# Optimization experiments

Hardware: AMD Instinct MI355X
Metric: run time of the kernel (lower is better)

## Reference

```python
import jax, jax.numpy as jnp
import numpy as np

N_NODES = 100000
N_EDGES = 1600000
IN_FEATS = 64
HIDDEN = 64
TOPO_DIM = 16
NUM_CLASSES = 4
NUM_GRAPHS = 64


def setup_inputs() -> dict:
    key = jax.random.key(0)
    ks = jax.random.split(key, 10)
    x = jax.random.normal(ks[0], (N_NODES, IN_FEATS), dtype=jnp.float32)
    edge_index = jax.random.randint(ks[1], (2, N_EDGES), 0, N_NODES, dtype=jnp.int64)
    batch = jnp.sort(jax.random.randint(ks[2], (N_NODES,), 0, NUM_GRAPHS, dtype=jnp.int64))
    topo = jax.random.normal(ks[3], (NUM_GRAPHS, TOPO_DIM), dtype=jnp.float32)
    # GCNConv weights (glorot-ish scale) and biases
    W1 = jax.random.normal(ks[4], (IN_FEATS, HIDDEN), dtype=jnp.float32) / np.sqrt(IN_FEATS)
    b1 = jnp.zeros((HIDDEN,), dtype=jnp.float32)
    W2 = jax.random.normal(ks[5], (HIDDEN, HIDDEN), dtype=jnp.float32) / np.sqrt(HIDDEN)
    b2 = jnp.zeros((HIDDEN,), dtype=jnp.float32)
    Wlin = jax.random.normal(ks[6], (HIDDEN + TOPO_DIM, NUM_CLASSES), dtype=jnp.float32) / np.sqrt(HIDDEN + TOPO_DIM)
    blin = jnp.zeros((NUM_CLASSES,), dtype=jnp.float32)
    return {"x": x, "edge_index": edge_index, "batch": batch, "topo": topo,
            "W1": W1, "b1": b1, "W2": W2, "b2": b2, "Wlin": Wlin, "blin": blin}


def _gcn_conv(x, W, b, src, dst, deg_inv_sqrt):
    # PyG GCNConv: add self-loops, symmetric normalization D^-1/2 (A+I) D^-1/2, then linear.
    xw = x @ W                                   # [N, H]
    norm = deg_inv_sqrt[src] * deg_inv_sqrt[dst]  # [E]
    msgs = xw[src] * norm[:, None]               # gather + scale, [E, H]
    agg = jax.ops.segment_sum(msgs, dst, num_segments=x.shape[0])
    # self-loop contribution: norm_ii = deg_inv_sqrt[i]^2
    agg = agg + xw * (deg_inv_sqrt * deg_inv_sqrt)[:, None]
    return agg + b


def reference(x, edge_index, batch, topo, W1, b1, W2, b2, Wlin, blin):
    src, dst = edge_index[0], edge_index[1]
    n = x.shape[0]
    # degree including self-loop
    deg = jax.ops.segment_sum(jnp.ones_like(dst, dtype=x.dtype), dst, num_segments=n) + 1.0
    deg_inv_sqrt = jax.lax.rsqrt(deg)
    h = jax.nn.relu(_gcn_conv(x, W1, b1, src, dst, deg_inv_sqrt))
    # F.dropout(p=0.5, training=False) -> identity at inference
    h = jax.nn.relu(_gcn_conv(h, W2, b2, src, dst, deg_inv_sqrt))
    # global mean pool over graphs
    sums = jax.ops.segment_sum(h, batch, num_segments=NUM_GRAPHS)
    counts = jax.ops.segment_sum(jnp.ones((n,), dtype=h.dtype), batch, num_segments=NUM_GRAPHS)
    g = sums / jnp.maximum(counts, 1.0)[:, None]  # [G, H]
    gtopo = jnp.concatenate([g, topo], axis=1)    # [G, H + topo_dim]
    return gtopo @ Wlin + blin
```

## Files before the change

### kernel.cpp

```cpp
#include <hip/hip_runtime.h>
#include <hip/hip_bf16.h>

#define NGRAPH  64
#define TOPO_D  16
#define NBLK    512
#define MAXB    512
#define GROWS   8

typedef float v2f __attribute__((ext_vector_type(2)));

static __device__ __forceinline__ unsigned f2bf(float f) {
    unsigned u = __float_as_uint(f);
    return (u + 0x7FFFu + ((u >> 16) & 1u)) >> 16;
}
static __device__ __forceinline__ float bf_lo(unsigned u) { return __uint_as_float(u << 16); }
static __device__ __forceinline__ float bf_hi(unsigned u) { return __uint_as_float(u & 0xFFFF0000u); }

static __device__ __forceinline__ void gemm_rows_bf(
        const float* __restrict__ X, const float* Wreg,
        unsigned short* __restrict__ Abf, int row0, int N, int lane) {
    #pragma unroll
    for (int j = 0; j < GROWS; ++j) {
        int row = row0 + j;
        if (row >= N) return;
        const float* xr = X + (size_t)row * 64;
        float acc = 0.0f;
        #pragma unroll
        for (int k = 0; k < 64; ++k) acc = fmaf(xr[k], Wreg[k], acc);
        Abf[(size_t)row * 64 + lane] = (unsigned short)f2bf(acc);
    }
}

static __device__ __forceinline__ void gemm_rows_fp8(
        const unsigned* __restrict__ X32, const float* Wreg,
        unsigned* __restrict__ A8, const float* __restrict__ dis,
        int row0, int N, int lane) {
    #pragma unroll
    for (int j = 0; j < GROWS; ++j) {
        int row = row0 + j;
        if (row >= N) return;
        const unsigned* xr = X32 + (size_t)row * 32;
        float acc = 0.0f;
        #pragma unroll
        for (int k = 0; k < 32; ++k) {
            unsigned u = xr[k];
            acc = fmaf(bf_lo(u), Wreg[2 * k], acc);
            acc = fmaf(bf_hi(u), Wreg[2 * k + 1], acc);
        }
        acc *= dis[row];
        float nb1 = __shfl_xor(acc, 1, 64);
        float lo = (lane & 1) ? nb1 : acc;
        float hi = (lane & 1) ? acc : nb1;
        int pk = __builtin_amdgcn_cvt_pk_fp8_f32(lo, hi, 0, false);
        int pk2 = __shfl_xor(pk, 2, 64);
        unsigned dw = (lane & 2) ? (((unsigned)pk2 & 0xFFFFu) | ((unsigned)pk << 16))
                                 : (((unsigned)pk & 0xFFFFu) | ((unsigned)pk2 << 16));
        if ((lane & 3) == 0) A8[(size_t)row * 16 + (lane >> 2)] = dw;
    }
}

__global__ __launch_bounds__(256) void hybrid_gemm_hist_kernel(
        const float* __restrict__ X, const float* __restrict__ W,
        unsigned short* __restrict__ Abf,
        const int* __restrict__ dst, int* __restrict__ bhist,
        int N, int E, int Gg, int nb2, int CE) {
    __shared__ int hist[MAXB];
    int t = threadIdx.x;
    if ((int)blockIdx.x < Gg) {
        int lane = t & 63;
        float Wreg[64];
        #pragma unroll
        for (int k = 0; k < 64; ++k) Wreg[k] = W[k * 64 + lane];
        int wave = __builtin_amdgcn_readfirstlane(blockIdx.x * 4 + (t >> 6));
        gemm_rows_bf(X, Wreg, Abf, wave * GROWS, N, lane);
    } else {
        int blk = blockIdx.x - Gg;
        for (int i = t; i < nb2; i += 256) hist[i] = 0;
        __syncthreads();
        int e0 = blk * CE, e1 = min(e0 + CE, E);
        for (int e = e0 + t; e < e1; e += 256) atomicAdd(&hist[dst[e] >> 8], 1);
        __syncthreads();
        for (int i = t; i < nb2; i += 256) bhist[blk * nb2 + i] = hist[i];
    }
}

__global__ __launch_bounds__(256) void scan_cols_kernel(
        int* __restrict__ bhist, int* __restrict__ ctot, int nb2) {
    __shared__ int sd[256];
    int c = blockIdx.x;
    int t = threadIdx.x;
    int v0 = bhist[t * nb2 + c];
    int v1 = bhist[(t + 256) * nb2 + c];
    int tsum = v0 + v1;
    sd[t] = tsum; __syncthreads();
    for (int off = 1; off < 256; off <<= 1) {
        int u = (t >= off) ? sd[t - off] : 0;
        __syncthreads();
        sd[t] += u;
        __syncthreads();
    }
    int excl = sd[t] - tsum;
    bhist[t * nb2 + c] = excl;
    bhist[(t + 256) * nb2 + c] = excl + v0;
    if (t == 255) ctot[c] = sd[255];
}

__global__ void scan_gstart_kernel(const int* __restrict__ ctot, int* __restrict__ cbase,
                                   const int* __restrict__ batch, int* __restrict__ gstart,
                                   int nb2, int N) {
    if (blockIdx.x == 0) {
        int lane = threadIdx.x;
        if (lane >= 64) return;
        int base = lane * 8;
        int vals[8];
        int s = 0;
        #pragma unroll
        for (int k = 0; k < 8; ++k) {
            int i = base + k;
            int v = (i < nb2) ? ctot[i] : 0;
            vals[k] = s; s += v;
        }
        int inc = s;
        for (int off = 1; off < 64; off <<= 1) {
            int u = __shfl_up(inc, off, 64);
            if (lane >= off) inc += u;
        }
        int lexcl = inc - s;
        #pragma unroll
        for (int k = 0; k < 8; ++k) {
            int i = base + k;
            if (i <= nb2) cbase[i] = lexcl + vals[k];
        }
    } else {
        int g = threadIdx.x;
        if (g > NGRAPH) return;
        int lo = 0, hi = N;
        while (lo < hi) {
            int mid = (lo + hi) >> 1;
            if (batch[mid] < g) lo = mid + 1; else hi = mid;
        }
        gstart[g] = lo;
    }
}

__global__ __launch_bounds__(256) void scatter_sorted_kernel(
        const int* __restrict__ src, const int* __restrict__ dst,
        const int* __restrict__ bhist, const int* __restrict__ cbase,
        unsigned* __restrict__ ebuf, int E, int nb2, int CE) {
    __shared__ int cur[MAXB];
    int blk = blockIdx.x, t = threadIdx.x;
    for (int i = t; i < nb2; i += 256) cur[i] = bhist[blk * nb2 + i] + cbase[i];
    __syncthreads();
    int e0 = blk * CE, e1 = min(e0 + CE, E);
    for (int e = e0 + t; e < e1; e += 256) {
        int d = dst[e];
        int pos = atomicAdd(&cur[d >> 8], 1);
        ebuf[pos] = ((unsigned)src[e] << 8) | (unsigned)(d & 255);
    }
}

__global__ __launch_bounds__(256) void build_csr_kernel(
        const unsigned* __restrict__ ebuf, const int* __restrict__ cbase,
        int* __restrict__ col, int* __restrict__ rowptr,
        int* __restrict__ degi, float* __restrict__ dis,
        const unsigned* __restrict__ Abf32, unsigned* __restrict__ A8, int N) {
    __shared__ int cnt[256];
    __shared__ int loff[256];
    __shared__ float disS[256];
    int b = blockIdx.x, t = threadIdx.x;
    int e0 = cbase[b], e1 = cbase[b + 1];
    cnt[t] = 0; __syncthreads();
    for (int i = e0 + t; i < e1; i += 256) atomicAdd(&cnt[ebuf[i] & 255u], 1);
    __syncthreads();
    int v = cnt[t];
    loff[t] = v; __syncthreads();
    for (int off = 1; off < 256; off <<= 1) {
        int u = (t >= off) ? loff[t - off] : 0;
        __syncthreads();
        loff[t] += u;
        __syncthreads();
    }
    int excl = loff[t] - v;
    int node = b * 256 + t;
    float ds = rsqrtf((float)v + 1.0f);
    disS[t] = ds;
    if (node < N) {
        degi[node]   = v;
        dis[node]    = ds;
        rowptr[node] = e0 + excl;
    }
    __syncthreads();
    cnt[t] = excl;
    __syncthreads();
    for (int i = e0 + t; i < e1; i += 256) {
        unsigned p = ebuf[i];
        int pos = atomicAdd(&cnt[p & 255u], 1);
        col[e0 + pos] = (int)(p >> 8);
    }
    int base8 = b * 256 * 16;
    for (int i = t; i < 256 * 16; i += 256) {
        int r = i >> 4;
        int dwo = i & 15;
        int nd = b * 256 + r;
        if (nd < N) {
            float d2 = disS[r];
            unsigned u0 = Abf32[(size_t)nd * 32 + dwo * 2];
            unsigned u1 = Abf32[(size_t)nd * 32 + dwo * 2 + 1];
            int dw = __builtin_amdgcn_cvt_pk_fp8_f32(bf_lo(u0) * d2, bf_hi(u0) * d2, 0, false);
            dw = __builtin_amdgcn_cvt_pk_fp8_f32(bf_lo(u1) * d2, bf_hi(u1) * d2, dw, true);
            A8[base8 + i] = (unsigned)dw;
        }
    }
}

static __device__ __forceinline__ void gather_node(
        const unsigned* __restrict__ A8, const int* __restrict__ col,
        int beg, int deg, int node, int f8, float acc[8]) {
    const char* Abase = (const char*)A8 + f8 * 8;
    uint2 an = *(const uint2*)(Abase + ((size_t)node << 6));
    v2f a0 = __builtin_amdgcn_cvt_pk_f32_fp8(an.x, false);
    v2f a1 = __builtin_amdgcn_cvt_pk_f32_fp8(an.x, true);
    v2f a2 = __builtin_amdgcn_cvt_pk_f32_fp8(an.y, false);
    v2f a3 = __builtin_amdgcn_cvt_pk_f32_fp8(an.y, true);
    acc[0] = a0.x; acc[1] = a0.y; acc[2] = a1.x; acc[3] = a1.y;
    acc[4] = a2.x; acc[5] = a2.y; acc[6] = a3.x; acc[7] = a3.y;
    int j = 0;
    for (; j + 4 <= deg; j += 4) {
        int s0 = col[beg + j]     << 6;
        int s1 = col[beg + j + 1] << 6;
        int s2 = col[beg + j + 2] << 6;
        int s3 = col[beg + j + 3] << 6;
        uint2 v0 = *(const uint2*)(Abase + s0);
        uint2 v1 = *(const uint2*)(Abase + s1);
        uint2 v2 = *(const uint2*)(Abase + s2);
        uint2 v3 = *(const uint2*)(Abase + s3);
        v2f f0, f1, f2, f3;
        f0 = __builtin_amdgcn_cvt_pk_f32_fp8(v0.x, false); acc[0] += f0.x; acc[1] += f0.y;
        f1 = __builtin_amdgcn_cvt_pk_f32_fp8(v0.x, true);  acc[2] += f1.x; acc[3] += f1.y;
        f2 = __builtin_amdgcn_cvt_pk_f32_fp8(v0.y, false); acc[4] += f2.x; acc[5] += f2.y;
        f3 = __builtin_amdgcn_cvt_pk_f32_fp8(v0.y, true);  acc[6] += f3.x; acc[7] += f3.y;
        f0 = __builtin_amdgcn_cvt_pk_f32_fp8(v1.x, false); acc[0] += f0.x; acc[1] += f0.y;
        f1 = __builtin_amdgcn_cvt_pk_f32_fp8(v1.x, true);  acc[2] += f1.x; acc[3] += f1.y;
        f2 = __builtin_amdgcn_cvt_pk_f32_fp8(v1.y, false); acc[4] += f2.x; acc[5] += f2.y;
        f3 = __builtin_amdgcn_cvt_pk_f32_fp8(v1.y, true);  acc[6] += f3.x; acc[7] += f3.y;
        f0 = __builtin_amdgcn_cvt_pk_f32_fp8(v2.x, false); acc[0] += f0.x; acc[1] += f0.y;
        f1 = __builtin_amdgcn_cvt_pk_f32_fp8(v2.x, true);  acc[2] += f1.x; acc[3] += f1.y;
        f2 = __builtin_amdgcn_cvt_pk_f32_fp8(v2.y, false); acc[4] += f2.x; acc[5] += f2.y;
        f3 = __builtin_amdgcn_cvt_pk_f32_fp8(v2.y, true);  acc[6] += f3.x; acc[7] += f3.y;
        f0 = __builtin_amdgcn_cvt_pk_f32_fp8(v3.x, false); acc[0] += f0.x; acc[1] += f0.y;
        f1 = __builtin_amdgcn_cvt_pk_f32_fp8(v3.x, true);  acc[2] += f1.x; acc[3] += f1.y;
        f2 = __builtin_amdgcn_cvt_pk_f32_fp8(v3.y, false); acc[4] += f2.x; acc[5] += f2.y;
        f3 = __builtin_amdgcn_cvt_pk_f32_fp8(v3.y, true);  acc[6] += f3.x; acc[7] += f3.y;
    }
    for (; j < deg; ++j) {
        int s = col[beg + j] << 6;
        uint2 v = *(const uint2*)(Abase + s);
        v2f f0 = __builtin_amdgcn_cvt_pk_f32_fp8(v.x, false);
        v2f f1 = __builtin_amdgcn_cvt_pk_f32_fp8(v.x, true);
        v2f f2 = __builtin_amdgcn_cvt_pk_f32_fp8(v.y, false);
        v2f f3 = __builtin_amdgcn_cvt_pk_f32_fp8(v.y, true);
        acc[0] += f0.x; acc[1] += f0.y; acc[2] += f1.x; acc[3] += f1.y;
        acc[4] += f2.x; acc[5] += f2.y; acc[6] += f3.x; acc[7] += f3.y;
    }
}

__global__ __launch_bounds__(256) void pull_csr_kernel(
        const unsigned* __restrict__ A8, unsigned* __restrict__ Bbf,
        const int* __restrict__ rowptr, const int* __restrict__ degi,
        const float* __restrict__ dis, const float* __restrict__ bias,
        const int* __restrict__ col, int N) {
    int wave = (blockIdx.x * blockDim.x + threadIdx.x) >> 6;
    int lane = threadIdx.x & 63;
    int i = lane >> 3;
    int f8 = lane & 7;
    int node = wave * 8 + i;
    bool valid = node < N;
    if (!valid) node = N - 1;
    int deg = degi[node];
    int beg = rowptr[node];
    float acc[8];
    gather_node(A8, col, beg, deg, node, f8, acc);
    float d = dis[node];
    float4 b0 = ((const float4*)bias)[f8 * 2];
    float4 b1 = ((const float4*)bias)[f8 * 2 + 1];
    float r0 = fmaxf(d * acc[0] + b0.x, 0.f);
    float r1 = fmaxf(d * acc[1] + b0.y, 0.f);
    float r2 = fmaxf(d * acc[2] + b0.z, 0.f);
    float r3 = fmaxf(d * acc[3] + b0.w, 0.f);
    float r4 = fmaxf(d * acc[4] + b1.x, 0.f);
    float r5 = fmaxf(d * acc[5] + b1.y, 0.f);
    float r6 = fmaxf(d * acc[6] + b1.z, 0.f);
    float r7 = fmaxf(d * acc[7] + b1.w, 0.f);
    if (valid) {
        uint4 o;
        o.x = f2bf(r0) | (f2bf(r1) << 16);
        o.y = f2bf(r2) | (f2bf(r3) << 16);
        o.z = f2bf(r4) | (f2bf(r5) << 16);
        o.w = f2bf(r6) | (f2bf(r7) << 16);
        *(uint4*)(Bbf + (size_t)node * 32 + f8 * 4) = o;
    }
}

__global__ __launch_bounds__(256) void gemm_scale_kernel(
        const unsigned* __restrict__ X32, const float* __restrict__ W,
        const float* __restrict__ dis, unsigned* __restrict__ A8, int N) {
    int lane = threadIdx.x & 63;
    float Wreg[64];
    #pragma unroll
    for (int k = 0; k < 64; ++k) Wreg[k] = W[k * 64 + lane];
    int wave = __builtin_amdgcn_readfirstlane(blockIdx.x * 4 + (threadIdx.x >> 6));
    gemm_rows_fp8(X32, Wreg, A8, dis, wave * GROWS, N, lane);
}

__global__ __launch_bounds__(256) void pull2_pool_kernel(
        const unsigned* __restrict__ A8, const int* __restrict__ rowptr,
        const int* __restrict__ degi, const float* __restrict__ dis,
        const float* __restrict__ bias, const int* __restrict__ col,
        const int* __restrict__ batch, float* __restrict__ gsum, int N) {
    __shared__ float hred[32][65];
    int wave = (blockIdx.x * blockDim.x + threadIdx.x) >> 6;
    int lane = threadIdx.x & 63;
    int w = threadIdx.x >> 6;
    int i = lane >> 3;
    int f8 = lane & 7;
    int node = wave * 8 + i;
    bool valid = node < N;
    if (!valid) node = N - 1;
    int deg = degi[node];
    int beg = rowptr[node];
    float acc[8];
    gather_node(A8, col, beg, deg, node, f8, acc);
    float d = dis[node];
    float4 b0 = ((const float4*)bias)[f8 * 2];
    float4 b1 = ((const float4*)bias)[f8 * 2 + 1];
    float h0 = fmaxf(d * acc[0] + b0.x, 0.f);
    float h1 = fmaxf(d * acc[1] + b0.y, 0.f);
    float h2 = fmaxf(d * acc[2] + b0.z, 0.f);
    float h3 = fmaxf(d * acc[3] + b0.w, 0.f);
    float h4 = fmaxf(d * acc[4] + b1.x, 0.f);
    float h5 = fmaxf(d * acc[5] + b1.y, 0.f);
    float h6 = fmaxf(d * acc[6] + b1.z, 0.f);
    float h7 = fmaxf(d * acc[7] + b1.w, 0.f);
    if (!valid) { h0 = 0.f; h1 = 0.f; h2 = 0.f; h3 = 0.f; h4 = 0.f; h5 = 0.f; h6 = 0.f; h7 = 0.f; }
    float* hp = &hred[w * 8 + i][f8 * 8];
    hp[0] = h0; hp[1] = h1; hp[2] = h2; hp[3] = h3;
    hp[4] = h4; hp[5] = h5; hp[6] = h6; hp[7] = h7;
    __syncthreads();
    int t = threadIdx.x;
    if (t < 64) {
        int nodeA = blockIdx.x * 32;
        int nodeB = min(nodeA + 31, N - 1);
        int gA = batch[min(nodeA, N - 1)];
        int gB = batch[nodeB];
        if (gA == gB) {
            float s = 0.f;
            #pragma unroll
            for (int r = 0; r < 32; ++r) s += hred[r][t];
            unsafeAtomicAdd(&gsum[gA * 64 + t], s);
        } else {
            for (int r = 0; r < 32; ++r) {
                int nd = nodeA + r;
                if (nd < N) unsafeAtomicAdd(&gsum[batch[nd] * 64 + t], hred[r][t]);
            }
        }
    }
}

__global__ __launch_bounds__(256) void head_kernel(
        const float* __restrict__ gsum, const int* __restrict__ gstart,
        const float* __restrict__ topo, const float* __restrict__ Wlin,
        const float* __restrict__ blin, float* __restrict__ out) {
    int t = threadIdx.x;
    int g = t >> 2;
    int c = t & 3;
    float cntf = (float)(gstart[g + 1] - gstart[g]);
    float inv = 1.0f / fmaxf(cntf, 1.0f);
    float v = blin[c];
    #pragma unroll
    for (int f = 0; f < 64; ++f) v += gsum[g * 64 + f] * inv * Wlin[f * 4 + c];
    #pragma unroll
    for (int t2 = 0; t2 < TOPO_D; ++t2) v += topo[g * TOPO_D + t2] * Wlin[(64 + t2) * 4 + c];
    out[g * 4 + c] = v;
}

extern "C" void kernel_launch(void* const* d_in, const int* in_sizes, int n_in,
                              void* d_out, int out_size, void* d_ws, size_t ws_size,
                              hipStream_t stream) {
    const float* x     = (const float*)d_in[0];
    const int*   ei    = (const int*)d_in[1];
    const int*   batch = (const int*)d_in[2];
    const float* topo  = (const float*)d_in[3];
    const float* W1    = (const float*)d_in[4];
    const float* b1    = (const float*)d_in[5];
    const float* W2    = (const float*)d_in[6];
    const float* b2    = (const float*)d_in[7];
    const float* Wlin  = (const float*)d_in[8];
    const float* blin  = (const float*)d_in[9];
    float* out = (float*)d_out;

    const int N = in_sizes[0] / 64;
    const int E = in_sizes[1] / 2;
    const int* src = ei;
    const int* dst = ei + E;
    const int nb2 = (N + 255) / 256;
    const int CE  = (E + NBLK - 1) / NBLK;

    char* ws = (char*)d_ws;
    size_t off = 0;
    unsigned short* Abf = (unsigned short*)(ws + off); off += (size_t)N * 64 * 2;
    unsigned* Bbf    = (unsigned*)(ws + off); off += (size_t)N * 32 * 4;
    unsigned* A8     = (unsigned*)(ws + off); off += (size_t)N * 64;
    int*      col    = (int*)     (ws + off); off += (size_t)E * 4;
    unsigned* ebuf   = (unsigned*)(ws + off); off += (size_t)E * 4;
    int*      bhist  = (int*)     (ws + off); off += (size_t)NBLK * nb2 * 4;
    int*      ctot   = (int*)     (ws + off); off += (size_t)(nb2 + 8) * 4;
    int*      cbase  = (int*)     (ws + off); off += (size_t)(nb2 + 8) * 4;
    int*      rowptr = (int*)     (ws + off); off += (size_t)(N + 1) * 4;
    int*      degi   = (int*)     (ws + off); off += (size_t)N * 4;
    float*    dis    = (float*)   (ws + off); off += (size_t)N * 4;
    int*      gstart = (int*)     (ws + off); off += (size_t)(NGRAPH + 8) * 4;
    float*    gsum   = (float*)   (ws + off); off += (size_t)NGRAPH * 64 * 4;

    hipMemsetAsync(gsum, 0, (size_t)NGRAPH * 64 * 4, stream);

    const int nWaves = (N + GROWS - 1) / GROWS;
    const int Gg = (nWaves + 3) / 4;
    hybrid_gemm_hist_kernel<<<Gg + NBLK, 256, 0, stream>>>(x, W1, Abf, dst, bhist, N, E, Gg, nb2, CE);
    scan_cols_kernel<<<nb2, 256, 0, stream>>>(bhist, ctot, nb2);
    scan_gstart_kernel<<<2, 256, 0, stream>>>(ctot, cbase, batch, gstart, nb2, N);
    scatter_sorted_kernel<<<NBLK, 256, 0, stream>>>(src, dst, bhist, cbase, ebuf, E, nb2, CE);
    build_csr_kernel<<<nb2, 256, 0, stream>>>(ebuf, cbase, col, rowptr, degi, dis,
                                              (const unsigned*)Abf, A8, N);

    int pullBlocks = ((N + 7) / 8 + 3) / 4;
    pull_csr_kernel<<<pullBlocks, 256, 0, stream>>>(A8, Bbf, rowptr, degi, dis, b1, col, N);

    gemm_scale_kernel<<<Gg, 256, 0, stream>>>(Bbf, W2, dis, A8, N);
    pull2_pool_kernel<<<pullBlocks, 256, 0, stream>>>(A8, rowptr, degi, dis, b2, col,
                                                      batch, gsum, N);

    head_kernel<<<1, 256, 0, stream>>>(gsum, gstart, topo, Wlin, blin, out);
}
```

Baseline: 235.3 us.

## Reorder layer-2 as aggregate-then-transform and fuse W2 GEMM into pull-pool kernel

```diff
diff --git a/kernel.cpp b/kernel.cpp
--- a/kernel.cpp
+++ b/kernel.cpp
@@ -28,34 +28,6 @@
         #pragma unroll
         for (int k = 0; k < 64; ++k) acc = fmaf(xr[k], Wreg[k], acc);
         Abf[(size_t)row * 64 + lane] = (unsigned short)f2bf(acc);
-    }
-}
-
-static __device__ __forceinline__ void gemm_rows_fp8(
-        const unsigned* __restrict__ X32, const float* Wreg,
-        unsigned* __restrict__ A8, const float* __restrict__ dis,
-        int row0, int N, int lane) {
-    #pragma unroll
-    for (int j = 0; j < GROWS; ++j) {
-        int row = row0 + j;
-        if (row >= N) return;
-        const unsigned* xr = X32 + (size_t)row * 32;
-        float acc = 0.0f;
-        #pragma unroll
-        for (int k = 0; k < 32; ++k) {
-            unsigned u = xr[k];
-            acc = fmaf(bf_lo(u), Wreg[2 * k], acc);
-            acc = fmaf(bf_hi(u), Wreg[2 * k + 1], acc);
-        }
-        acc *= dis[row];
-        float nb1 = __shfl_xor(acc, 1, 64);
-        float lo = (lane & 1) ? nb1 : acc;
-        float hi = (lane & 1) ? acc : nb1;
-        int pk = __builtin_amdgcn_cvt_pk_fp8_f32(lo, hi, 0, false);
-        int pk2 = __shfl_xor(pk, 2, 64);
-        unsigned dw = (lane & 2) ? (((unsigned)pk2 & 0xFFFFu) | ((unsigned)pk << 16))
-                                 : (((unsigned)pk & 0xFFFFu) | ((unsigned)pk2 << 16));
-        if ((lane & 3) == 0) A8[(size_t)row * 16 + (lane >> 2)] = dw;
     }
 }
 
@@ -107,7 +79,7 @@
 
 __global__ void scan_gstart_kernel(const int* __restrict__ ctot, int* __restrict__ cbase,
                                    const int* __restrict__ batch, int* __restrict__ gstart,
-                                   int nb2, int N) {
+                                   float* __restrict__ gsum, int nb2, int N) {
     if (blockIdx.x == 0) {
         int lane = threadIdx.x;
         if (lane >= 64) return;
@@ -131,7 +103,7 @@
             int i = base + k;
             if (i <= nb2) cbase[i] = lexcl + vals[k];
         }
-    } else {
+    } else if (blockIdx.x == 1) {
         int g = threadIdx.x;
         if (g > NGRAPH) return;
         int lo = 0, hi = N;
@@ -140,6 +112,8 @@
             if (batch[mid] < g) lo = mid + 1; else hi = mid;
         }
         gstart[g] = lo;
+    } else {
+        for (int i = threadIdx.x; i < NGRAPH * 64; i += 256) gsum[i] = 0.f;
     }
 }
 
@@ -265,7 +239,7 @@
 }
 
 __global__ __launch_bounds__(256) void pull_csr_kernel(
-        const unsigned* __restrict__ A8, unsigned* __restrict__ Bbf,
+        const unsigned* __restrict__ A8, unsigned* __restrict__ C8,
         const int* __restrict__ rowptr, const int* __restrict__ degi,
         const float* __restrict__ dis, const float* __restrict__ bias,
         const int* __restrict__ col, int N) {
@@ -292,35 +266,32 @@
     float r6 = fmaxf(d * acc[6] + b1.z, 0.f);
     float r7 = fmaxf(d * acc[7] + b1.w, 0.f);
     if (valid) {
-        uint4 o;
-        o.x = f2bf(r0) | (f2bf(r1) << 16);
-        o.y = f2bf(r2) | (f2bf(r3) << 16);
-        o.z = f2bf(r4) | (f2bf(r5) << 16);
-        o.w = f2bf(r6) | (f2bf(r7) << 16);
-        *(uint4*)(Bbf + (size_t)node * 32 + f8 * 4) = o;
-    }
-}
-
-__global__ __launch_bounds__(256) void gemm_scale_kernel(
-        const unsigned* __restrict__ X32, const float* __restrict__ W,
-        const float* __restrict__ dis, unsigned* __restrict__ A8, int N) {
-    int lane = threadIdx.x & 63;
-    float Wreg[64];
-    #pragma unroll
-    for (int k = 0; k < 64; ++k) Wreg[k] = W[k * 64 + lane];
-    int wave = __builtin_amdgcn_readfirstlane(blockIdx.x * 4 + (threadIdx.x >> 6));
-    gemm_rows_fp8(X32, Wreg, A8, dis, wave * GROWS, N, lane);
+        int p0 = __builtin_amdgcn_cvt_pk_fp8_f32(d * r0, d * r1, 0, false);
+        p0 = __builtin_amdgcn_cvt_pk_fp8_f32(d * r2, d * r3, p0, true);
+        int p1 = __builtin_amdgcn_cvt_pk_fp8_f32(d * r4, d * r5, 0, false);
+        p1 = __builtin_amdgcn_cvt_pk_fp8_f32(d * r6, d * r7, p1, true);
+        uint2 o; o.x = (unsigned)p0; o.y = (unsigned)p1;
+        *(uint2*)((char*)C8 + ((size_t)node << 6) + (f8 << 3)) = o;
+    }
 }
 
 __global__ __launch_bounds__(256) void pull2_pool_kernel(
-        const unsigned* __restrict__ A8, const int* __restrict__ rowptr,
+        const unsigned* __restrict__ C8, const int* __restrict__ rowptr,
         const int* __restrict__ degi, const float* __restrict__ dis,
         const float* __restrict__ bias, const int* __restrict__ col,
-        const int* __restrict__ batch, float* __restrict__ gsum, int N) {
-    __shared__ float hred[32][65];
-    int wave = (blockIdx.x * blockDim.x + threadIdx.x) >> 6;
-    int lane = threadIdx.x & 63;
-    int w = threadIdx.x >> 6;
+        const int* __restrict__ batch, const float* __restrict__ W2,
+        float* __restrict__ gsum, int N) {
+    __shared__ float w2s[4096];
+    __shared__ float sred[32][72];
+    __shared__ float red[4][65];
+    int t = threadIdx.x;
+    ((float4*)w2s)[t]       = ((const float4*)W2)[t];
+    ((float4*)w2s)[t + 256] = ((const float4*)W2)[t + 256];
+    ((float4*)w2s)[t + 512] = ((const float4*)W2)[t + 512];
+    ((float4*)w2s)[t + 768] = ((const float4*)W2)[t + 768];
+    int wave = (blockIdx.x * blockDim.x + t) >> 6;
+    int lane = t & 63;
+    int w = t >> 6;
     int i = lane >> 3;
     int f8 = lane & 7;
     int node = wave * 8 + i;
@@ -329,40 +300,81 @@
     int deg = degi[node];
     int beg = rowptr[node];
     float acc[8];
-    gather_node(A8, col, beg, deg, node, f8, acc);
-    float d = dis[node];
-    float4 b0 = ((const float4*)bias)[f8 * 2];
-    float4 b1 = ((const float4*)bias)[f8 * 2 + 1];
-    float h0 = fmaxf(d * acc[0] + b0.x, 0.f);
-    float h1 = fmaxf(d * acc[1] + b0.y, 0.f);
-    float h2 = fmaxf(d * acc[2] + b0.z, 0.f);
-    float h3 = fmaxf(d * acc[3] + b0.w, 0.f);
-    float h4 = fmaxf(d * acc[4] + b1.x, 0.f);
-    float h5 = fmaxf(d * acc[5] + b1.y, 0.f);
-    float h6 = fmaxf(d * acc[6] + b1.z, 0.f);
-    float h7 = fmaxf(d * acc[7] + b1.w, 0.f);
-    if (!valid) { h0 = 0.f; h1 = 0.f; h2 = 0.f; h3 = 0.f; h4 = 0.f; h5 = 0.f; h6 = 0.f; h7 = 0.f; }
-    float* hp = &hred[w * 8 + i][f8 * 8];
-    hp[0] = h0; hp[1] = h1; hp[2] = h2; hp[3] = h3;
-    hp[4] = h4; hp[5] = h5; hp[6] = h6; hp[7] = h7;
+    gather_node(C8, col, beg, deg, node, f8, acc);
+    float* sp = &sred[w * 8 + i][f8 * 8];
+    sp[0] = acc[0]; sp[1] = acc[1]; sp[2] = acc[2]; sp[3] = acc[3];
+    sp[4] = acc[4]; sp[5] = acc[5]; sp[6] = acc[6]; sp[7] = acc[7];
     __syncthreads();
-    int t = threadIdx.x;
-    if (t < 64) {
-        int nodeA = blockIdx.x * 32;
-        int nodeB = min(nodeA + 31, N - 1);
-        int gA = batch[min(nodeA, N - 1)];
-        int gB = batch[nodeB];
-        if (gA == gB) {
-            float s = 0.f;
-            #pragma unroll
-            for (int r = 0; r < 32; ++r) s += hred[r][t];
+    float g0 = 0.f, g1 = 0.f, g2 = 0.f, g3 = 0.f, g4 = 0.f, g5 = 0.f, g6 = 0.f, g7 = 0.f;
+    #pragma unroll
+    for (int kc = 0; kc < 16; ++kc) {
+        float wa = w2s[(kc * 4 + 0) * 64 + lane];
+        float wb = w2s[(kc * 4 + 1) * 64 + lane];
+        float wc = w2s[(kc * 4 + 2) * 64 + lane];
+        float wd = w2s[(kc * 4 + 3) * 64 + lane];
+        float4 sv;
+        sv = *(const float4*)&sred[w * 8 + 0][kc * 4];
+        g0 = fmaf(sv.x, wa, fmaf(sv.y, wb, fmaf(sv.z, wc, fmaf(sv.w, wd, g0))));
+        sv = *(const float4*)&sred[w * 8 + 1][kc * 4];
+        g1 = fmaf(sv.x, wa, fmaf(sv.y, wb, fmaf(sv.z, wc, fmaf(sv.w, wd, g1))));
+        sv = *(const float4*)&sred[w * 8 + 2][kc * 4];
+        g2 = fmaf(sv.x, wa, fmaf(sv.y, wb, fmaf(sv.z, wc, fmaf(sv.w, wd, g2))));
+        sv = *(const float4*)&sred[w * 8 + 3][kc * 4];
+        g3 = fmaf(sv.x, wa, fmaf(sv.y, wb, fmaf(sv.z, wc, fmaf(sv.w, wd, g3))));
+        sv = *(const float4*)&sred[w * 8 + 4][kc * 4];
+        g4 = fmaf(sv.x, wa, fmaf(sv.y, wb, fmaf(sv.z, wc, fmaf(sv.w, wd, g4))));
+        sv = *(const float4*)&sred[w * 8 + 5][kc * 4];
+        g5 = fmaf(sv.x, wa, fmaf(sv.y, wb, fmaf(sv.z, wc, fmaf(sv.w, wd, g5))));
+        sv = *(const float4*)&sred[w * 8 + 6][kc * 4];
+        g6 = fmaf(sv.x, wa, fmaf(sv.y, wb, fmaf(sv.z, wc, fmaf(sv.w, wd, g6))));
+        sv = *(const float4*)&sred[w * 8 + 7][kc * 4];
+        g7 = fmaf(sv.x, wa, fmaf(sv.y, wb, fmaf(sv.z, wc, fmaf(sv.w, wd, g7))));
+    }
+    int base = (blockIdx.x * 4 + w) * 8;
+    float d0 = dis[min(base + 0, N - 1)];
+    float d1 = dis[min(base + 1, N - 1)];
+    float d2 = dis[min(base + 2, N - 1)];
+    float d3 = dis[min(base + 3, N - 1)];
+    float d4 = dis[min(base + 4, N - 1)];
+    float d5 = dis[min(base + 5, N - 1)];
+    float d6 = dis[min(base + 6, N - 1)];
+    float d7 = dis[min(base + 7, N - 1)];
+    float bf = bias[lane];
+    float h0 = fmaxf(fmaf(d0, g0, bf), 0.f);
+    float h1 = fmaxf(fmaf(d1, g1, bf), 0.f);
+    float h2 = fmaxf(fmaf(d2, g2, bf), 0.f);
+    float h3 = fmaxf(fmaf(d3, g3, bf), 0.f);
+    float h4 = fmaxf(fmaf(d4, g4, bf), 0.f);
+    float h5 = fmaxf(fmaf(d5, g5, bf), 0.f);
+    float h6 = fmaxf(fmaf(d6, g6, bf), 0.f);
+    float h7 = fmaxf(fmaf(d7, g7, bf), 0.f);
+    if (base + 0 >= N) h0 = 0.f;
+    if (base + 1 >= N) h1 = 0.f;
+    if (base + 2 >= N) h2 = 0.f;
+    if (base + 3 >= N) h3 = 0.f;
+    if (base + 4 >= N) h4 = 0.f;
+    if (base + 5 >= N) h5 = 0.f;
+    if (base + 6 >= N) h6 = 0.f;
+    if (base + 7 >= N) h7 = 0.f;
+    int nodeA = blockIdx.x * 32;
+    int gA = batch[min(nodeA, N - 1)];
+    int gB = batch[min(nodeA + 31, N - 1)];
+    if (gA == gB) {
+        red[w][lane] = h0 + h1 + h2 + h3 + h4 + h5 + h6 + h7;
+        __syncthreads();
+        if (t < 64) {
+            float s = red[0][t] + red[1][t] + red[2][t] + red[3][t];
             unsafeAtomicAdd(&gsum[gA * 64 + t], s);
-        } else {
-            for (int r = 0; r < 32; ++r) {
-                int nd = nodeA + r;
-                if (nd < N) unsafeAtomicAdd(&gsum[batch[nd] * 64 + t], hred[r][t]);
-            }
-        }
+        }
+    } else {
+        int q0 = batch[min(base + 0, N - 1)]; unsafeAtomicAdd(&gsum[q0 * 64 + lane], h0);
+        int q1 = batch[min(base + 1, N - 1)]; unsafeAtomicAdd(&gsum[q1 * 64 + lane], h1);
+        int q2 = batch[min(base + 2, N - 1)]; unsafeAtomicAdd(&gsum[q2 * 64 + lane], h2);
+        int q3 = batch[min(base + 3, N - 1)]; unsafeAtomicAdd(&gsum[q3 * 64 + lane], h3);
+        int q4 = batch[min(base + 4, N - 1)]; unsafeAtomicAdd(&gsum[q4 * 64 + lane], h4);
+        int q5 = batch[min(base + 5, N - 1)]; unsafeAtomicAdd(&gsum[q5 * 64 + lane], h5);
+        int q6 = batch[min(base + 6, N - 1)]; unsafeAtomicAdd(&gsum[q6 * 64 + lane], h6);
+        int q7 = batch[min(base + 7, N - 1)]; unsafeAtomicAdd(&gsum[q7 * 64 + lane], h7);
     }
 }
 
@@ -408,8 +420,8 @@
     char* ws = (char*)d_ws;
     size_t off = 0;
     unsigned short* Abf = (unsigned short*)(ws + off); off += (size_t)N * 64 * 2;
-    unsigned* Bbf    = (unsigned*)(ws + off); off += (size_t)N * 32 * 4;
     unsigned* A8     = (unsigned*)(ws + off); off += (size_t)N * 64;
+    unsigned* C8     = (unsigned*)(ws + off); off += (size_t)N * 64;
     int*      col    = (int*)     (ws + off); off += (size_t)E * 4;
     unsigned* ebuf   = (unsigned*)(ws + off); off += (size_t)E * 4;
     int*      bhist  = (int*)     (ws + off); off += (size_t)NBLK * nb2 * 4;
@@ -421,23 +433,20 @@
     int*      gstart = (int*)     (ws + off); off += (size_t)(NGRAPH + 8) * 4;
     float*    gsum   = (float*)   (ws + off); off += (size_t)NGRAPH * 64 * 4;
 
-    hipMemsetAsync(gsum, 0, (size_t)NGRAPH * 64 * 4, stream);
-
     const int nWaves = (N + GROWS - 1) / GROWS;
     const int Gg = (nWaves + 3) / 4;
     hybrid_gemm_hist_kernel<<<Gg + NBLK, 256, 0, stream>>>(x, W1, Abf, dst, bhist, N, E, Gg, nb2, CE);
     scan_cols_kernel<<<nb2, 256, 0, stream>>>(bhist, ctot, nb2);
-    scan_gstart_kernel<<<2, 256, 0, stream>>>(ctot, cbase, batch, gstart, nb2, N);
+    scan_gstart_kernel<<<3, 256, 0, stream>>>(ctot, cbase, batch, gstart, gsum, nb2, N);
     scatter_sorted_kernel<<<NBLK, 256, 0, stream>>>(src, dst, bhist, cbase, ebuf, E, nb2, CE);
     build_csr_kernel<<<nb2, 256, 0, stream>>>(ebuf, cbase, col, rowptr, degi, dis,
                                               (const unsigned*)Abf, A8, N);
 
     int pullBlocks = ((N + 7) / 8 + 3) / 4;
-    pull_csr_kernel<<<pullBlocks, 256, 0, stream>>>(A8, Bbf, rowptr, degi, dis, b1, col, N);
-
-    gemm_scale_kernel<<<Gg, 256, 0, stream>>>(Bbf, W2, dis, A8, N);
-    pull2_pool_kernel<<<pullBlocks, 256, 0, stream>>>(A8, rowptr, degi, dis, b2, col,
-                                                      batch, gsum, N);
+    pull_csr_kernel<<<pullBlocks, 256, 0, stream>>>(A8, C8, rowptr, degi, dis, b1, col, N);
+
+    pull2_pool_kernel<<<pullBlocks, 256, 0, stream>>>(C8, rowptr, degi, dis, b2, col,
+                                                      batch, W2, gsum, N);
 
     head_kernel<<<1, 256, 0, stream>>>(gsum, gstart, topo, Wlin, blin, out);
 }
```

After: 215.9 us. 1.09x faster.
